# Kernel optimization log

Hardware: AMD Instinct MI355X
Metric: run time of the kernel (lower is better)

## Reference

```python
import jax, jax.numpy as jnp
import numpy as np
from jax import lax

H = 64          # num_heads
P = 64          # head_dim
N = 128         # ssm_state_size
G = 8           # n_groups
K = 4           # conv_kernel
D_MODEL = 4096  # hidden_size
I = H * P                      # intermediate_size = 4096
GN = G * N                     # groups_time_state_size = 1024
CONV_DIM = I + 2 * GN          # 6144
PROJ = I + CONV_DIM + H        # 10304
EPS = 1e-5
GROUP_SIZE = I // G            # 512


def setup_inputs() -> dict:
    key = jax.random.key(0)
    ks = jax.random.split(key, 6)
    B, L = 2, 2048
    s = 0.02
    return {
        "hidden_states": jax.random.normal(ks[0], (B, L, D_MODEL), jnp.float32),
        "in_proj_w": jax.random.normal(ks[1], (PROJ, D_MODEL), jnp.float32) * s,
        "conv_weight": jax.random.normal(ks[2], (CONV_DIM, K), jnp.float32) * s,
        "conv_bias": jnp.zeros((CONV_DIM,), jnp.float32),
        "dt_bias": jnp.ones((H,), jnp.float32),
        "A_log": jnp.log(jnp.arange(1, H + 1, dtype=jnp.float32)),
        "D": jnp.ones((H,), jnp.float32),
        "norm_weight": jnp.ones((I,), jnp.float32),
        "out_proj_w": jax.random.normal(ks[3], (D_MODEL, I), jnp.float32) * s,
    }


def reference(hidden_states, in_proj_w, conv_weight, conv_bias, dt_bias, A_log, D, norm_weight, out_proj_w):
    B, L, _ = hidden_states.shape

    # in_proj, then split into gate / conv-stream / dt
    proj = jnp.einsum("bld,pd->blp", hidden_states, in_proj_w)
    gate = proj[..., :I]
    hbc = proj[..., I:I + CONV_DIM]          # (B, L, conv_dim), pre-conv
    dt = proj[..., -H:]                       # (B, L, H)

    # depthwise causal conv1d + SiLU
    pad = jnp.pad(hbc, ((0, 0), (K - 1, 0), (0, 0)))
    conv = conv_bias
    for k in range(K):  # K=4, tiny fixed loop
        conv = conv + pad[:, k:k + L, :] * conv_weight[:, k]
    xBC = jax.nn.silu(conv)

    x = xBC[..., :I].reshape(B, L, H, P)                        # (B,L,H,P)
    Bm = xBC[..., I:I + GN].reshape(B, L, G, N)
    Cm = xBC[..., I + GN:].reshape(B, L, G, N)
    hpg = H // G
    B_h = jnp.repeat(Bm, hpg, axis=2)                            # (B,L,H,N)
    C_h = jnp.repeat(Cm, hpg, axis=2)                            # (B,L,H,N)

    # dt processing: softplus(dt + dt_bias), limits (0, inf)
    dt_p = jax.nn.softplus(dt + dt_bias)                         # (B,L,H)
    A = -jnp.exp(A_log)                                          # (H,)
    dA = jnp.exp(dt_p * A)                                       # (B,L,H)
    dtx = dt_p[..., None] * x                                    # (B,L,H,P)

    # selective scan over sequence (O(L)), state: (B,H,P,N)
    def step(state, inp):
        dA_t, dtx_t, B_t, C_t = inp
        state = state * dA_t[..., None, None] + dtx_t[..., None] * B_t[:, :, None, :]
        y_t = jnp.einsum("bhpn,bhn->bhp", state, C_t)
        return state, y_t

    xs = (jnp.moveaxis(dA, 1, 0), jnp.moveaxis(dtx, 1, 0),
          jnp.moveaxis(B_h, 1, 0), jnp.moveaxis(C_h, 1, 0))
    state0 = jnp.zeros((B, H, P, N), jnp.float32)
    final_state, ys = lax.scan(step, state0, xs)
    y = jnp.moveaxis(ys, 0, 1) + x * D[None, None, :, None]      # (B,L,H,P)
    y = y.reshape(B, L, I)

    # gated grouped RMSNorm: 8 independent RMSNorms over 512 elems each
    yg = y.reshape(B, L, G, GROUP_SIZE)
    var = jnp.mean(yg * yg, axis=-1, keepdims=True)
    yn = (yg * lax.rsqrt(var + EPS)).reshape(B, L, I) * norm_weight
    yn = yn * jax.nn.silu(gate)

    out = jnp.einsum("bli,di->bld", yn, out_proj_w)

    conv_state_new = jnp.moveaxis(hbc[:, L - (K - 1):, :], 1, 2)  # (B, conv_dim, K-1)
    return out, conv_state_new, final_state
```

## Files before the change

kernel.cpp:

```cpp
#include <hip/hip_runtime.h>
#include <cstdint>
#include <cstddef>

typedef __bf16 bf16;
typedef float f32x4 __attribute__((ext_vector_type(4)));
typedef bf16 bf16x8 __attribute__((ext_vector_type(8)));
typedef bf16 bf16x4 __attribute__((ext_vector_type(4)));

#define DM    4096
#define LL    2048
#define BB    2
#define BT    4096
#define II    4096
#define GN_   1024
#define CONVD 6144
#define PROJD 10304
#define NPAD  10496
#define HH    64
#define PP    64
#define NN    128
#define CT    64
#define NC    32

#define OUT_OFS_CONV  16777216
#define OUT_OFS_STATE 16814080

#define WS_HSB    0UL
#define WS_WINB   33554432UL
#define WS_DSB    0UL
#define WS_PROJ   119537664UL
#define WS_XBC    291504128UL
#define WS_DTDA   392167424UL
#define WS_Y      394264576UL
#define WS_WOUTB  0UL
#define WS_YNB    33554432UL

__device__ __forceinline__ void gl2lds16(const void* g, void* l) {
  __builtin_amdgcn_global_load_lds(
      (__attribute__((address_space(1))) unsigned int*)(uintptr_t)g,
      (__attribute__((address_space(3))) unsigned int*)(uintptr_t)l, 16, 0, 0);
}

__global__ __launch_bounds__(256) void cast_kernel(const float* __restrict__ src,
                                                   bf16* __restrict__ dst,
                                                   long nsrc, long ndst) {
  long i = ((long)blockIdx.x * 256 + threadIdx.x) * 4;
  if (i >= ndst) return;
  bf16x4 o;
  if (i < nsrc) {
    float4 v = *(const float4*)(src + i);
    o[0] = (bf16)v.x; o[1] = (bf16)v.y; o[2] = (bf16)v.z; o[3] = (bf16)v.w;
  } else {
    o[0] = (bf16)0.f; o[1] = (bf16)0.f; o[2] = (bf16)0.f; o[3] = (bf16)0.f;
  }
  *(bf16x4*)(dst + i) = o;
}

#define BARF() do { asm volatile("" ::: "memory");                    \
                    __builtin_amdgcn_s_barrier();                     \
                    asm volatile("" ::: "memory"); } while (0)
#define WAITLGKM0() do { asm volatile("s_waitcnt lgkmcnt(0)" ::: "memory"); \
                         __builtin_amdgcn_sched_barrier(0); } while (0)
#define WAITVM(n) asm volatile("s_waitcnt vmcnt(" #n ")" ::: "memory")
#define PRIO1 __builtin_amdgcn_s_setprio(1)
#define PRIO0 __builtin_amdgcn_s_setprio(0)

__device__ __forceinline__ void stage_A_half(const bf16* __restrict__ A, int K,
                                             int arow, int kt, bf16* lds,
                                             int h, int tid) {
#pragma unroll
  for (int j = 0; j < 2; ++j) {
    const int r  = h * 64 + j * 128 + (tid >> 3);
    const int cb = (tid & 7) * 16;
    const int cs = cb ^ ((r & 7) << 4);
    gl2lds16(A + (size_t)(arow + r) * K + kt * 64 + (cs >> 1),
             lds + r * 64 + (cb >> 1));
  }
}
__device__ __forceinline__ void stage_B_half(const bf16* __restrict__ B, int K,
                                             int brow, int kt, bf16* lds,
                                             int h, int tid) {
#pragma unroll
  for (int j = 0; j < 2; ++j) {
    const int quarter = j * 2 + (tid >> 8);
    const int kq = tid & 255;
    const int r  = quarter * 64 + h * 32 + (kq >> 3);
    const int cb = (kq & 7) * 16;
    const int cs = cb ^ ((r & 7) << 4);
    gl2lds16(B + (size_t)(brow + r) * K + kt * 64 + (cs >> 1),
             lds + r * 64 + (cb >> 1));
  }
}

#define LDA4(p, mh) do {                                                     \
  _Pragma("unroll") for (int mt = 0; mt < 4; ++mt)                           \
  _Pragma("unroll") for (int kk = 0; kk < 2; ++kk) {                         \
    const int rr = wm * 128 + (mh) * 64 + mt * 16 + l16;                     \
    const int cc = (kk * 64 + quad * 16) ^ ((rr & 7) << 4);                  \
    a_[mt][kk] = *(const bf16x8*)((const char*)(&sA[p][rr][0]) + cc);        \
  } } while (0)

#define LDB2(p, np, barr) do {                                               \
  _Pragma("unroll") for (int nt = 0; nt < 2; ++nt)                           \
  _Pragma("unroll") for (int kk = 0; kk < 2; ++kk) {                         \
    const int rr = wn * 64 + (np) * 32 + nt * 16 + l16;                      \
    const int cc = (kk * 64 + quad * 16) ^ ((rr & 7) << 4);                  \
    barr[nt][kk] = *(const bf16x8*)((const char*)(&sB[p][rr][0]) + cc);      \
  } } while (0)

#define MFMAQ(mh, barr, nb0) do {                                            \
  _Pragma("unroll") for (int kk = 0; kk < 2; ++kk)                           \
  _Pragma("unroll") for (int mt = 0; mt < 4; ++mt)                           \
  _Pragma("unroll") for (int nt = 0; nt < 2; ++nt)                           \
    acc[(mh) * 4 + mt][(nb0) + nt] = __builtin_amdgcn_mfma_f32_16x16x32_bf16(\
        a_[mt][kk], barr[nt][kk], acc[(mh) * 4 + mt][(nb0) + nt], 0, 0, 0);  \
  } while (0)

__global__ __launch_bounds__(512, 2) void gemm256(const bf16* __restrict__ A,
                                                  const bf16* __restrict__ B,
                                                  float* __restrict__ C,
                                                  int M, int N, int K, int NB) {
  __shared__ __align__(16) bf16 sA[2][256][64];
  __shared__ __align__(16) bf16 sB[2][256][64];

  const int tid  = threadIdx.x;
  const int wave = tid >> 6, lane = tid & 63;
  const int l16  = lane & 15, quad = lane >> 4;
  const int wm   = wave >> 2, wn = wave & 3;

  const int nwg = gridDim.x;
  const int q = nwg >> 3, r8 = nwg & 7;
  const int xcd = blockIdx.x & 7, idx = blockIdx.x >> 3;
  const int wgid = (xcd < r8 ? xcd * (q + 1) : r8 * (q + 1) + (xcd - r8) * q) + idx;
  const int mb = wgid / NB, nb = wgid - mb * NB;
  const int arow = mb * 256, brow = nb * 256;

  f32x4 acc[8][4];
#pragma unroll
  for (int i = 0; i < 8; ++i)
#pragma unroll
    for (int j = 0; j < 4; ++j) acc[i][j] = (f32x4)0.f;

  const int NT = K >> 6;

  stage_A_half(A, K, arow, 0, &sA[0][0][0], 0, tid);
  stage_B_half(B, K, brow, 0, &sB[0][0][0], 0, tid);
  stage_A_half(A, K, arow, 0, &sA[0][0][0], 1, tid);
  stage_B_half(B, K, brow, 0, &sB[0][0][0], 1, tid);
  stage_A_half(A, K, arow, 1, &sA[1][0][0], 0, tid);
  stage_B_half(B, K, brow, 1, &sB[1][0][0], 0, tid);
  stage_A_half(A, K, arow, 1, &sA[1][0][0], 1, tid);
  WAITVM(6);
  BARF();

  bf16x8 a_[4][2], b0_[2][2], b1_[2][2];

  for (int i = 0; i < NT / 2; ++i) {
    const int t1o = 2 * i + 1;
    const int t2  = (2 * i + 2 < NT) ? 2 * i + 2 : NT - 1;
    const int t3  = (2 * i + 3 < NT) ? 2 * i + 3 : NT - 1;

    LDA4(0, 0); LDB2(0, 0, b0_);
    stage_B_half(B, K, brow, t1o, &sB[1][0][0], 1, tid);
    BARF(); WAITLGKM0();
    PRIO1; MFMAQ(0, b0_, 0); PRIO0;
    BARF();
    LDB2(0, 1, b1_);
    stage_A_half(A, K, arow, t2, &sA[0][0][0], 0, tid);
    BARF(); WAITLGKM0();
    PRIO1; MFMAQ(0, b1_, 2); PRIO0;
    BARF();
    LDA4(0, 1);
    stage_B_half(B, K, brow, t2, &sB[0][0][0], 0, tid);
    BARF(); WAITLGKM0();
    PRIO1; MFMAQ(1, b1_, 2); PRIO0;
    BARF();
    stage_A_half(A, K, arow, t2, &sA[0][0][0], 1, tid);
    WAITVM(6);
    BARF();
    PRIO1; MFMAQ(1, b0_, 0); PRIO0;
    BARF();
    LDA4(1, 0); LDB2(1, 0, b0_);
    stage_B_half(B, K, brow, t2, &sB[0][0][0], 1, tid);
    BARF(); WAITLGKM0();
    PRIO1; MFMAQ(0, b0_, 0); PRIO0;
    BARF();
    LDB2(1, 1, b1_);
    stage_A_half(A, K, arow, t3, &sA[1][0][0], 0, tid);
    BARF(); WAITLGKM0();
    PRIO1; MFMAQ(0, b1_, 2); PRIO0;
    BARF();
    LDA4(1, 1);
    stage_B_half(B, K, brow, t3, &sB[1][0][0], 0, tid);
    BARF(); WAITLGKM0();
    PRIO1; MFMAQ(1, b1_, 2); PRIO0;
    BARF();
    stage_A_half(A, K, arow, t3, &sA[1][0][0], 1, tid);
    WAITVM(6);
    BARF();
    PRIO1; MFMAQ(1, b0_, 0); PRIO0;
    BARF();
  }
  asm volatile("s_waitcnt vmcnt(0)" ::: "memory");
  __builtin_amdgcn_s_barrier();

#pragma unroll
  for (int mt = 0; mt < 8; ++mt) {
    const int row0 = arow + wm * 128 + mt * 16 + quad * 4;
#pragma unroll
    for (int nt = 0; nt < 4; ++nt) {
      const int col = brow + wn * 64 + nt * 16 + l16;
#pragma unroll
      for (int r = 0; r < 4; ++r)
        C[(size_t)(row0 + r) * N + col] = acc[mt][nt][r];
    }
  }
}

#define CTILE 64
__global__ __launch_bounds__(256) void conv_kernel(const float* __restrict__ proj,
                                                   const float* __restrict__ cw,
                                                   const float* __restrict__ cb,
                                                   bf16* __restrict__ xbc) {
  const int c   = blockIdx.x * 256 + threadIdx.x;
  const int bt0 = blockIdx.y * CTILE;
  const int t0  = bt0 & (LL - 1);
  const float4 w = *(const float4*)(cw + c * 4);
  const float bias = cb[c];
  const float* p = proj + (size_t)bt0 * NPAD + II + c;
  float h0, h1, h2;
  if (t0 == 0) {
    h0 = 0.f; h1 = 0.f; h2 = 0.f;
  } else {
    h0 = p[-3 * (ptrdiff_t)NPAD];
    h1 = p[-2 * (ptrdiff_t)NPAD];
    h2 = p[-(ptrdiff_t)NPAD];
  }
  bf16* q = xbc + (size_t)bt0 * CONVD + c;
#pragma unroll 8
  for (int t = 0; t < CTILE; ++t) {
    const float cur = p[(ptrdiff_t)t * NPAD];
    const float acc = bias + h0 * w.x + h1 * w.y + h2 * w.z + cur * w.w;
    q[(size_t)t * CONVD] = (bf16)(acc / (1.f + __expf(-acc)));
    h0 = h1; h1 = h2; h2 = cur;
  }
}

__global__ __launch_bounds__(256) void dt_kernel(const float* __restrict__ proj,
                                                 const float* __restrict__ dt_bias,
                                                 const float* __restrict__ A_log,
                                                 float* __restrict__ dtda) {
  const int idx = blockIdx.x * 256 + threadIdx.x;
  const int bt = idx >> 6, h = idx & 63;
  const float z = proj[(size_t)bt * NPAD + (II + CONVD) + h] + dt_bias[h];
  const float sp = (z > 20.f) ? z : log1pf(__expf(z));
  const float a = -__expf(A_log[h]);
  float2 o; o.x = sp; o.y = __expf(sp * a);
  *(float2*)(dtda + (size_t)idx * 2) = o;
}

__global__ __launch_bounds__(256) void convstate_kernel(const float* __restrict__ proj,
                                                        float* __restrict__ outp) {
  const int idx = blockIdx.x * 256 + threadIdx.x;
  if (idx >= BB * CONVD * 3) return;
  const int b = idx / (CONVD * 3);
  const int r = idx - b * CONVD * 3;
  const int c = r / 3, j = r - c * 3;
  outp[idx] = proj[((size_t)b * LL + (LL - 3 + j)) * NPAD + II + c];
}

__global__ __launch_bounds__(256) void chunkA_kernel(const bf16* __restrict__ xbc,
                                                     const float* __restrict__ dtda,
                                                     const float* __restrict__ A_log,
                                                     float* __restrict__ ybuf,
                                                     bf16* __restrict__ dsb) {
  const int h = blockIdx.x, c = blockIdx.y, b = blockIdx.z;
  const int g = h >> 3;
  const int tid = threadIdx.x;
  const int wave = tid >> 6, lane = tid & 63;
  const int l16 = lane & 15, quad = lane >> 4;

  __shared__ __align__(16) bf16 CsBt[8192];
  __shared__ __align__(16) bf16 Bs[64][128];
  __shared__ __align__(16) bf16 Xt[64][64];
  __shared__ __align__(16) bf16 Ws[64][64];
  __shared__ float cums[64], dtps[64], wls[64];

  bf16 (*Cs)[128] = (bf16(*)[128])CsBt;
  bf16 (*Bt)[64]  = (bf16(*)[64])CsBt;

  const size_t rowbase = ((size_t)b * LL + (size_t)c * CT) * CONVD;

  {
    const int i = tid >> 2, col0 = (tid & 3) * 32;
    const bf16* gpC = xbc + rowbase + (size_t)i * CONVD + (II + GN_) + g * 128 + col0;
    const bf16* gpB = xbc + rowbase + (size_t)i * CONVD + II + g * 128 + col0;
    const int sx = i & 15;
#pragma unroll
    for (int k = 0; k < 4; ++k) {
      const int n0 = col0 + k * 8;
      const int eo = ((n0 >> 3) ^ sx) * 8;
      *(bf16x8*)(&Cs[i][0] + eo) = *(const bf16x8*)(gpC + k * 8);
      *(bf16x8*)(&Bs[i][0] + eo) = *(const bf16x8*)(gpB + k * 8);
    }
  }
  {
    const int j = tid >> 2, p0 = (tid & 3) * 16;
    const bf16* gpX = xbc + rowbase + (size_t)j * CONVD + h * 64 + p0;
#pragma unroll
    for (int k = 0; k < 2; ++k) {
      bf16x8 v = *(const bf16x8*)(gpX + k * 8);
#pragma unroll
      for (int e = 0; e < 8; ++e) {
        const int pp = p0 + k * 8 + e;
        Xt[pp][(((j >> 3) ^ (pp & 7)) * 8) + (j & 7)] = v[e];
      }
    }
  }
  if (wave == 0) {
    const float Ah = -__expf(A_log[h]);
    float2 dd = *(const float2*)(dtda + ((size_t)((b * LL + c * CT + lane)) * 64 + h) * 2);
    float s = dd.x * Ah;
#pragma unroll
    for (int d = 1; d < 64; d <<= 1) {
      float v = __shfl_up(s, d);
      if (lane >= d) s += v;
    }
    const float tot = __shfl(s, 63);
    cums[lane] = s;
    dtps[lane] = dd.x;
    wls[lane]  = __expf(tot - s) * dd.x;
  }
  __syncthreads();

  const int mrow = wave * 16 + l16;
  {
    f32x4 accg[4];
#pragma unroll
    for (int nt = 0; nt < 4; ++nt) accg[nt] = (f32x4)0.f;
#pragma unroll
    for (int k0 = 0; k0 < 128; k0 += 32) {
      bf16x8 af = *(const bf16x8*)&Cs[mrow][(((k0 >> 3) + quad) ^ (mrow & 15)) * 8];
#pragma unroll
      for (int nt = 0; nt < 4; ++nt) {
        const int nrow = nt * 16 + l16;
        bf16x8 bfr = *(const bf16x8*)&Bs[nrow][(((k0 >> 3) + quad) ^ (nrow & 15)) * 8];
        accg[nt] = __builtin_amdgcn_mfma_f32_16x16x32_bf16(af, bfr, accg[nt], 0, 0, 0);
      }
    }
#pragma unroll
    for (int nt = 0; nt < 4; ++nt) {
      const int j = nt * 16 + l16;
#pragma unroll
      for (int r = 0; r < 4; ++r) {
        const int i = wave * 16 + quad * 4 + r;
        float v = 0.f;
        if (j <= i) v = accg[nt][r] * __expf(cums[i] - cums[j]) * dtps[j];
        Ws[i][(((j >> 3) ^ (i & 7)) * 8) + (j & 7)] = (bf16)v;
      }
    }
  }
  __syncthreads();

  {
    const int n = tid >> 1, j0 = (tid & 1) * 32;
#pragma unroll
    for (int jj = 0; jj < 32; ++jj) {
      const int j = j0 + jj;
      bf16 v = Bs[j][(((n >> 3) ^ (j & 15)) * 8) + (n & 7)];
      Bt[n][(((j >> 3) ^ (n & 7)) * 8) + (j & 7)] = v;
    }
  }
  __syncthreads();

  f32x4 accy[4];
#pragma unroll
  for (int pt = 0; pt < 4; ++pt) accy[pt] = (f32x4)0.f;
#pragma unroll
  for (int k0 = 0; k0 < 64; k0 += 32) {
    bf16x8 af = *(const bf16x8*)&Ws[mrow][(((k0 >> 3) + quad) ^ (mrow & 7)) * 8];
#pragma unroll
    for (int pt = 0; pt < 4; ++pt) {
      const int prow = pt * 16 + l16;
      bf16x8 bfr = *(const bf16x8*)&Xt[prow][(((k0 >> 3) + quad) ^ (prow & 7)) * 8];
      accy[pt] = __builtin_amdgcn_mfma_f32_16x16x32_bf16(af, bfr, accy[pt], 0, 0, 0);
    }
  }

  f32x4 accs[8];
#pragma unroll
  for (int nt = 0; nt < 8; ++nt) accs[nt] = (f32x4)0.f;
#pragma unroll
  for (int k0 = 0; k0 < 64; k0 += 32) {
    bf16x8 axr = *(const bf16x8*)&Xt[mrow][(((k0 >> 3) + quad) ^ (mrow & 7)) * 8];
    bf16x8 ax;
#pragma unroll
    for (int e = 0; e < 8; ++e)
      ax[e] = (bf16)((float)axr[e] * wls[k0 + quad * 8 + e]);
#pragma unroll
    for (int nt = 0; nt < 8; ++nt) {
      const int nrow = nt * 16 + l16;
      bf16x8 bfr = *(const bf16x8*)&Bt[nrow][(((k0 >> 3) + quad) ^ (nrow & 7)) * 8];
      accs[nt] = __builtin_amdgcn_mfma_f32_16x16x32_bf16(ax, bfr, accs[nt], 0, 0, 0);
    }
  }

#pragma unroll
  for (int pt = 0; pt < 4; ++pt) {
#pragma unroll
    for (int r = 0; r < 4; ++r) {
      const int i = wave * 16 + quad * 4 + r;
      ybuf[((size_t)(b * LL + c * CT + i)) * II + h * 64 + pt * 16 + l16] = accy[pt][r];
    }
  }
  const size_t dbase = (((size_t)(b * HH + h)) * NC + c) * (CT * NN);
#pragma unroll
  for (int nt = 0; nt < 8; ++nt) {
#pragma unroll
    for (int r = 0; r < 4; ++r) {
      const int p = wave * 16 + quad * 4 + r;
      dsb[dbase + (size_t)p * NN + nt * 16 + l16] = (bf16)accs[nt][r];
    }
  }
}

__global__ __launch_bounds__(256) void chain_kernel(const float* __restrict__ dtda,
                                                    const float* __restrict__ A_log,
                                                    bf16* __restrict__ dsb,
                                                    float* __restrict__ fst) {
  const int blk = blockIdx.x;
  const int b = blk >> 8, h = (blk >> 2) & 63, qtr = blk & 3;
  const int tid = threadIdx.x, wave = tid >> 6, lane = tid & 63;
  __shared__ float DcL[NC];

  const float Ah = -__expf(A_log[h]);
#pragma unroll
  for (int cc = 0; cc < 8; ++cc) {
    const int c = wave * 8 + cc;
    float2 dd = *(const float2*)(dtda + ((size_t)(b * LL + c * CT + lane) * 64 + h) * 2);
    float a = dd.x * Ah;
#pragma unroll
    for (int m = 1; m <= 32; m <<= 1) a += __shfl_xor(a, m);
    if (lane == 0) DcL[c] = __expf(a);
  }
  __syncthreads();

  const int local = qtr * 2048 + tid * 8;
  const size_t base = ((size_t)(b * HH + h)) * NC * (CT * NN) + local;
  float s[8];
#pragma unroll
  for (int e = 0; e < 8; ++e) s[e] = 0.f;

  for (int c = 0; c < NC; ++c) {
    bf16* p = dsb + base + (size_t)c * (CT * NN);
    bf16x8 d0 = *(const bf16x8*)(p);
    const float dc = DcL[c];
    bf16x8 o0;
#pragma unroll
    for (int e = 0; e < 8; ++e) o0[e] = (bf16)s[e];
    *(bf16x8*)(p) = o0;
#pragma unroll
    for (int e = 0; e < 8; ++e) s[e] = s[e] * dc + (float)d0[e];
  }
  float* fp = fst + ((size_t)(b * HH + h)) * (PP * NN) + local;
#pragma unroll
  for (int k = 0; k < 2; ++k) {
    float4 v = { s[k * 4], s[k * 4 + 1], s[k * 4 + 2], s[k * 4 + 3] };
    *(float4*)(fp + k * 4) = v;
  }
}

__global__ __launch_bounds__(256) void chunkB_kernel(const bf16* __restrict__ xbc,
                                                     const float* __restrict__ dtda,
                                                     const float* __restrict__ A_log,
                                                     const float* __restrict__ Dv,
                                                     const bf16* __restrict__ spb,
                                                     float* __restrict__ ybuf) {
  const int h = blockIdx.x, c = blockIdx.y, b = blockIdx.z;
  const int g = h >> 3;
  const int tid = threadIdx.x;
  const int wave = tid >> 6, lane = tid & 63;
  const int l16 = lane & 15, quad = lane >> 4;

  __shared__ __align__(16) bf16 Cs[64][128];
  __shared__ __align__(16) bf16 Sp[64][128];
  __shared__ float es[64];

  const size_t rowbase = ((size_t)b * LL + (size_t)c * CT) * CONVD;
  {
    const int i = tid >> 2, col0 = (tid & 3) * 32;
    const bf16* gpC = xbc + rowbase + (size_t)i * CONVD + (II + GN_) + g * 128 + col0;
    const int sx = i & 15;
#pragma unroll
    for (int k = 0; k < 4; ++k) {
      const int n0 = col0 + k * 8;
      *(bf16x8*)(&Cs[i][0] + (((n0 >> 3) ^ sx) * 8)) = *(const bf16x8*)(gpC + k * 8);
    }
  }
  {
    const int p = tid >> 2, nseg = (tid & 3) * 32;
    const bf16* gp = spb + (((size_t)(b * HH + h)) * NC + c) * (CT * NN) + (size_t)p * NN + nseg;
    const int sx = p & 15;
#pragma unroll
    for (int k = 0; k < 4; ++k) {
      const int n0 = nseg + k * 8;
      bf16x8 v = *(const bf16x8*)(gp + k * 8);
      *(bf16x8*)(&Sp[p][0] + (((n0 >> 3) ^ sx) * 8)) = v;
    }
  }
  if (wave == 0) {
    const float Ah = -__expf(A_log[h]);
    float2 dd = *(const float2*)(dtda + ((size_t)(b * LL + c * CT + lane) * 64 + h) * 2);
    float s = dd.x * Ah;
#pragma unroll
    for (int d = 1; d < 64; d <<= 1) {
      float v = __shfl_up(s, d);
      if (lane >= d) s += v;
    }
    es[lane] = __expf(s);
  }
  __syncthreads();

  const int mrow = wave * 16 + l16;
  f32x4 acc[4];
#pragma unroll
  for (int pt = 0; pt < 4; ++pt) acc[pt] = (f32x4)0.f;
#pragma unroll
  for (int k0 = 0; k0 < 128; k0 += 32) {
    bf16x8 af = *(const bf16x8*)&Cs[mrow][(((k0 >> 3) + quad) ^ (mrow & 15)) * 8];
#pragma unroll
    for (int pt = 0; pt < 4; ++pt) {
      const int prow = pt * 16 + l16;
      bf16x8 bfr = *(const bf16x8*)&Sp[prow][(((k0 >> 3) + quad) ^ (prow & 15)) * 8];
      acc[pt] = __builtin_amdgcn_mfma_f32_16x16x32_bf16(af, bfr, acc[pt], 0, 0, 0);
    }
  }

  const float Dh = Dv[h];
#pragma unroll
  for (int pt = 0; pt < 4; ++pt) {
#pragma unroll
    for (int r = 0; r < 4; ++r) {
      const int i = wave * 16 + quad * 4 + r;
      const int p = pt * 16 + l16;
      const size_t row = (size_t)(b * LL + c * CT + i);
      const size_t ya = row * II + h * 64 + p;
      const float xv = (float)xbc[row * CONVD + h * 64 + p];
      ybuf[ya] = acc[pt][r] * es[i] + ybuf[ya] + Dh * xv;
    }
  }
}

__global__ __launch_bounds__(256) void norm_kernel(const float* __restrict__ y,
                                                   const float* __restrict__ proj,
                                                   const float* __restrict__ nw,
                                                   bf16* __restrict__ yn) {
  const int bt = blockIdx.x, tid = threadIdx.x;
  const float* yr = y + (size_t)bt * II + tid * 16;
  float4 v[4];
  float ss = 0.f;
#pragma unroll
  for (int i = 0; i < 4; ++i) {
    v[i] = *(const float4*)(yr + i * 4);
    ss += v[i].x * v[i].x + v[i].y * v[i].y + v[i].z * v[i].z + v[i].w * v[i].w;
  }
#pragma unroll
  for (int m = 1; m <= 16; m <<= 1) ss += __shfl_xor(ss, m);
  const float rstd = rsqrtf(ss * (1.f / 512.f) + 1e-5f);

  const float* gr  = proj + (size_t)bt * NPAD + tid * 16;
  const float* nwr = nw + tid * 16;
  bf16x8 o0, o1;
#pragma unroll
  for (int i = 0; i < 4; ++i) {
    float4 gv = *(const float4*)(gr + i * 4);
    float4 nv = *(const float4*)(nwr + i * 4);
    const float* vv = (const float*)&v[i];
    const float* gg = (const float*)&gv;
    const float* nn = (const float*)&nv;
#pragma unroll
    for (int j = 0; j < 4; ++j) {
      const float gate = gg[j];
      const float val = vv[j] * rstd * nn[j] * (gate / (1.f + __expf(-gate)));
      if (i < 2) o0[i * 4 + j] = (bf16)val;
      else       o1[(i - 2) * 4 + j] = (bf16)val;
    }
  }
  bf16* dst = yn + (size_t)bt * II + tid * 16;
  *(bf16x8*)(dst)     = o0;
  *(bf16x8*)(dst + 8) = o1;
}

extern "C" void kernel_launch(void* const* d_in, const int* in_sizes, int n_in,
                              void* d_out, int out_size, void* d_ws, size_t ws_size,
                              hipStream_t stream) {
  const float* hs      = (const float*)d_in[0];
  const float* w_in    = (const float*)d_in[1];
  const float* cw      = (const float*)d_in[2];
  const float* cb      = (const float*)d_in[3];
  const float* dt_bias = (const float*)d_in[4];
  const float* A_log   = (const float*)d_in[5];
  const float* Dv      = (const float*)d_in[6];
  const float* nw      = (const float*)d_in[7];
  const float* w_out   = (const float*)d_in[8];

  char* ws = (char*)d_ws;
  bf16*  hsb   = (bf16*)(ws + WS_HSB);
  bf16*  winb  = (bf16*)(ws + WS_WINB);
  bf16*  dsb   = (bf16*)(ws + WS_DSB);
  float* proj  = (float*)(ws + WS_PROJ);
  bf16*  xbc   = (bf16*)(ws + WS_XBC);
  float* dtda  = (float*)(ws + WS_DTDA);
  float* ybuf  = (float*)(ws + WS_Y);
  bf16*  ynb   = (bf16*)(ws + WS_YNB);
  bf16*  woutb = (bf16*)(ws + WS_WOUTB);

  float* outp = (float*)d_out;

  cast_kernel<<<16384, 256, 0, stream>>>(hs, hsb, 16777216L, 16777216L);
  cast_kernel<<<41984, 256, 0, stream>>>(w_in, winb, (long)PROJD * DM, (long)NPAD * DM);

  gemm256<<<(BT / 256) * (NPAD / 256), 512, 0, stream>>>(hsb, winb, proj, BT, NPAD, DM, NPAD / 256);

  conv_kernel<<<dim3(CONVD / 256, BT / CTILE), 256, 0, stream>>>(proj, cw, cb, xbc);
  dt_kernel<<<(BT * HH) / 256, 256, 0, stream>>>(proj, dt_bias, A_log, dtda);
  convstate_kernel<<<(BB * CONVD * 3 + 255) / 256, 256, 0, stream>>>(proj, outp + OUT_OFS_CONV);

  chunkA_kernel<<<dim3(HH, NC, BB), 256, 0, stream>>>(xbc, dtda, A_log, ybuf, dsb);
  chain_kernel<<<BB * HH * 4, 256, 0, stream>>>(dtda, A_log, dsb, outp + OUT_OFS_STATE);
  chunkB_kernel<<<dim3(HH, NC, BB), 256, 0, stream>>>(xbc, dtda, A_log, Dv, dsb, ybuf);

  cast_kernel<<<16384, 256, 0, stream>>>(w_out, woutb, 16777216L, 16777216L);
  norm_kernel<<<BT, 256, 0, stream>>>(ybuf, proj, nw, ynb);

  gemm256<<<(BT / 256) * (DM / 256), 512, 0, stream>>>(ynb, woutb, outp, BT, DM, II, DM / 256);
}
```

Baseline: 974.2 us.

## Merge small kernels, remap scan blocks for L2 locality, use direct-to-LDS loads

Combines the two input casts into one launch and merges the dt and conv-state kernels, which cuts launch overhead. The chunk kernels now use a 1D grid decoded so blocks that share a group's B/C data run near each other, for better L2 reuse. Their B/C and state staging now goes through global_load_lds, and the B transpose writes 8-element vectors. The chain kernel prefetches the next chunk's state, and the GEMM gets an extra lgkmcnt wait hint. Several unrelated tweaks together, each with a small effect and some risk around LDS swizzle correctness.

```diff
diff --git a/kernel.cpp b/kernel.cpp
--- a/kernel.cpp
+++ b/kernel.cpp
@@ -41,6 +41,31 @@
       (__attribute__((address_space(3))) unsigned int*)(uintptr_t)l, 16, 0, 0);
 }
 
+__global__ __launch_bounds__(256) void cast2_kernel(const float* __restrict__ s1,
+                                                    bf16* __restrict__ d1,
+                                                    const float* __restrict__ s2,
+                                                    bf16* __restrict__ d2,
+                                                    long nsrc2, long ndst2) {
+  if (blockIdx.x < 16384) {
+    long i = ((long)blockIdx.x * 256 + threadIdx.x) * 4;
+    float4 v = *(const float4*)(s1 + i);
+    bf16x4 o;
+    o[0] = (bf16)v.x; o[1] = (bf16)v.y; o[2] = (bf16)v.z; o[3] = (bf16)v.w;
+    *(bf16x4*)(d1 + i) = o;
+  } else {
+    long i = ((long)(blockIdx.x - 16384) * 256 + threadIdx.x) * 4;
+    if (i >= ndst2) return;
+    bf16x4 o;
+    if (i < nsrc2) {
+      float4 v = *(const float4*)(s2 + i);
+      o[0] = (bf16)v.x; o[1] = (bf16)v.y; o[2] = (bf16)v.z; o[3] = (bf16)v.w;
+    } else {
+      o[0] = (bf16)0.f; o[1] = (bf16)0.f; o[2] = (bf16)0.f; o[3] = (bf16)0.f;
+    }
+    *(bf16x4*)(d2 + i) = o;
+  }
+}
+
 __global__ __launch_bounds__(256) void cast_kernel(const float* __restrict__ src,
                                                    bf16* __restrict__ dst,
                                                    long nsrc, long ndst) {
@@ -61,6 +86,7 @@
                     asm volatile("" ::: "memory"); } while (0)
 #define WAITLGKM0() do { asm volatile("s_waitcnt lgkmcnt(0)" ::: "memory"); \
                          __builtin_amdgcn_sched_barrier(0); } while (0)
+#define HINTLGKM8() asm volatile("s_waitcnt lgkmcnt(8)" ::: "memory")
 #define WAITVM(n) asm volatile("s_waitcnt vmcnt(" #n ")" ::: "memory")
 #define PRIO1 __builtin_amdgcn_s_setprio(1)
 #define PRIO0 __builtin_amdgcn_s_setprio(0)
@@ -162,6 +188,7 @@
 
     LDA4(0, 0); LDB2(0, 0, b0_);
     stage_B_half(B, K, brow, t1o, &sB[1][0][0], 1, tid);
+    HINTLGKM8();
     BARF(); WAITLGKM0();
     PRIO1; MFMAQ(0, b0_, 0); PRIO0;
     BARF();
@@ -182,6 +209,7 @@
     BARF();
     LDA4(1, 0); LDB2(1, 0, b0_);
     stage_B_half(B, K, brow, t2, &sB[0][0][0], 1, tid);
+    HINTLGKM8();
     BARF(); WAITLGKM0();
     PRIO1; MFMAQ(0, b0_, 0); PRIO0;
     BARF();
@@ -246,36 +274,43 @@
   }
 }
 
-__global__ __launch_bounds__(256) void dt_kernel(const float* __restrict__ proj,
-                                                 const float* __restrict__ dt_bias,
-                                                 const float* __restrict__ A_log,
-                                                 float* __restrict__ dtda) {
-  const int idx = blockIdx.x * 256 + threadIdx.x;
-  const int bt = idx >> 6, h = idx & 63;
-  const float z = proj[(size_t)bt * NPAD + (II + CONVD) + h] + dt_bias[h];
-  const float sp = (z > 20.f) ? z : log1pf(__expf(z));
-  const float a = -__expf(A_log[h]);
-  float2 o; o.x = sp; o.y = __expf(sp * a);
-  *(float2*)(dtda + (size_t)idx * 2) = o;
-}
-
-__global__ __launch_bounds__(256) void convstate_kernel(const float* __restrict__ proj,
-                                                        float* __restrict__ outp) {
-  const int idx = blockIdx.x * 256 + threadIdx.x;
-  if (idx >= BB * CONVD * 3) return;
-  const int b = idx / (CONVD * 3);
-  const int r = idx - b * CONVD * 3;
-  const int c = r / 3, j = r - c * 3;
-  outp[idx] = proj[((size_t)b * LL + (LL - 3 + j)) * NPAD + II + c];
-}
+__global__ __launch_bounds__(256) void dtcs_kernel(const float* __restrict__ proj,
+                                                   const float* __restrict__ dt_bias,
+                                                   const float* __restrict__ A_log,
+                                                   float* __restrict__ dtda,
+                                                   float* __restrict__ outp) {
+  const int bid = blockIdx.x;
+  if (bid < 1024) {
+    const int idx = bid * 256 + threadIdx.x;
+    const int bt = idx >> 6, h = idx & 63;
+    const float z = proj[(size_t)bt * NPAD + (II + CONVD) + h] + dt_bias[h];
+    const float sp = (z > 20.f) ? z : log1pf(__expf(z));
+    const float a = -__expf(A_log[h]);
+    float2 o; o.x = sp; o.y = __expf(sp * a);
+    *(float2*)(dtda + (size_t)idx * 2) = o;
+  } else {
+    const int idx = (bid - 1024) * 256 + threadIdx.x;
+    if (idx >= BB * CONVD * 3) return;
+    const int b = idx / (CONVD * 3);
+    const int r = idx - b * CONVD * 3;
+    const int c = r / 3, j = r - c * 3;
+    outp[idx] = proj[((size_t)b * LL + (LL - 3 + j)) * NPAD + II + c];
+  }
+}
+
+#define SCAN_DECODE()                                                  \
+  const int lin = blockIdx.x;                                          \
+  const int hh  = (lin >> 3) & 7;                                      \
+  const int id  = (lin & 7) | ((lin >> 6) << 3);                       \
+  const int g   = id >> 6, c = (id >> 1) & 31, b = id & 1;             \
+  const int h   = g * 8 + hh;
 
 __global__ __launch_bounds__(256) void chunkA_kernel(const bf16* __restrict__ xbc,
                                                      const float* __restrict__ dtda,
                                                      const float* __restrict__ A_log,
                                                      float* __restrict__ ybuf,
                                                      bf16* __restrict__ dsb) {
-  const int h = blockIdx.x, c = blockIdx.y, b = blockIdx.z;
-  const int g = h >> 3;
+  SCAN_DECODE();
   const int tid = threadIdx.x;
   const int wave = tid >> 6, lane = tid & 63;
   const int l16 = lane & 15, quad = lane >> 4;
@@ -292,16 +327,15 @@
   const size_t rowbase = ((size_t)b * LL + (size_t)c * CT) * CONVD;
 
   {
-    const int i = tid >> 2, col0 = (tid & 3) * 32;
-    const bf16* gpC = xbc + rowbase + (size_t)i * CONVD + (II + GN_) + g * 128 + col0;
-    const bf16* gpB = xbc + rowbase + (size_t)i * CONVD + II + g * 128 + col0;
-    const int sx = i & 15;
-#pragma unroll
-    for (int k = 0; k < 4; ++k) {
-      const int n0 = col0 + k * 8;
-      const int eo = ((n0 >> 3) ^ sx) * 8;
-      *(bf16x8*)(&Cs[i][0] + eo) = *(const bf16x8*)(gpC + k * 8);
-      *(bf16x8*)(&Bs[i][0] + eo) = *(const bf16x8*)(gpB + k * 8);
+    const int r0 = wave * 16;
+    const bf16* gC = xbc + rowbase + (II + GN_) + g * 128;
+    const bf16* gB = xbc + rowbase + II + g * 128;
+#pragma unroll
+    for (int j = 0; j < 4; ++j) {
+      const int r  = r0 + j * 4 + (lane >> 4);
+      const int ch = (lane & 15) ^ (r & 15);
+      gl2lds16(gC + (size_t)r * CONVD + ch * 8, &Cs[r0 + j * 4][0]);
+      gl2lds16(gB + (size_t)r * CONVD + ch * 8, &Bs[r0 + j * 4][0]);
     }
   }
   {
@@ -365,10 +399,14 @@
   {
     const int n = tid >> 1, j0 = (tid & 1) * 32;
 #pragma unroll
-    for (int jj = 0; jj < 32; ++jj) {
-      const int j = j0 + jj;
-      bf16 v = Bs[j][(((n >> 3) ^ (j & 15)) * 8) + (n & 7)];
-      Bt[n][(((j >> 3) ^ (n & 7)) * 8) + (j & 7)] = v;
+    for (int k = 0; k < 4; ++k) {
+      bf16x8 v;
+#pragma unroll
+      for (int e = 0; e < 8; ++e) {
+        const int j = j0 + k * 8 + e;
+        v[e] = Bs[j][(((n >> 3) ^ (j & 15)) * 8) + (n & 7)];
+      }
+      *(bf16x8*)(&Bt[n][((((j0 + k * 8) >> 3) ^ (n & 7)) * 8)]) = v;
     }
   }
   __syncthreads();
@@ -443,7 +481,6 @@
     for (int m = 1; m <= 32; m <<= 1) a += __shfl_xor(a, m);
     if (lane == 0) DcL[c] = __expf(a);
   }
-  __syncthreads();
 
   const int local = qtr * 2048 + tid * 8;
   const size_t base = ((size_t)(b * HH + h)) * NC * (CT * NN) + local;
@@ -451,9 +488,13 @@
 #pragma unroll
   for (int e = 0; e < 8; ++e) s[e] = 0.f;
 
+  bf16x8 d0 = *(const bf16x8*)(dsb + base);
+  __syncthreads();
+
   for (int c = 0; c < NC; ++c) {
     bf16* p = dsb + base + (size_t)c * (CT * NN);
-    bf16x8 d0 = *(const bf16x8*)(p);
+    bf16x8 dn;
+    if (c + 1 < NC) dn = *(const bf16x8*)(p + (CT * NN));
     const float dc = DcL[c];
     bf16x8 o0;
 #pragma unroll
@@ -461,6 +502,7 @@
     *(bf16x8*)(p) = o0;
 #pragma unroll
     for (int e = 0; e < 8; ++e) s[e] = s[e] * dc + (float)d0[e];
+    d0 = dn;
   }
   float* fp = fst + ((size_t)(b * HH + h)) * (PP * NN) + local;
 #pragma unroll
@@ -476,8 +518,7 @@
                                                      const float* __restrict__ Dv,
                                                      const bf16* __restrict__ spb,
                                                      float* __restrict__ ybuf) {
-  const int h = blockIdx.x, c = blockIdx.y, b = blockIdx.z;
-  const int g = h >> 3;
+  SCAN_DECODE();
   const int tid = threadIdx.x;
   const int wave = tid >> 6, lane = tid & 63;
   const int l16 = lane & 15, quad = lane >> 4;
@@ -488,24 +529,15 @@
 
   const size_t rowbase = ((size_t)b * LL + (size_t)c * CT) * CONVD;
   {
-    const int i = tid >> 2, col0 = (tid & 3) * 32;
-    const bf16* gpC = xbc + rowbase + (size_t)i * CONVD + (II + GN_) + g * 128 + col0;
-    const int sx = i & 15;
-#pragma unroll
-    for (int k = 0; k < 4; ++k) {
-      const int n0 = col0 + k * 8;
-      *(bf16x8*)(&Cs[i][0] + (((n0 >> 3) ^ sx) * 8)) = *(const bf16x8*)(gpC + k * 8);
-    }
-  }
-  {
-    const int p = tid >> 2, nseg = (tid & 3) * 32;
-    const bf16* gp = spb + (((size_t)(b * HH + h)) * NC + c) * (CT * NN) + (size_t)p * NN + nseg;
-    const int sx = p & 15;
-#pragma unroll
-    for (int k = 0; k < 4; ++k) {
-      const int n0 = nseg + k * 8;
-      bf16x8 v = *(const bf16x8*)(gp + k * 8);
-      *(bf16x8*)(&Sp[p][0] + (((n0 >> 3) ^ sx) * 8)) = v;
+    const int r0 = wave * 16;
+    const bf16* gC = xbc + rowbase + (II + GN_) + g * 128;
+    const bf16* gS = spb + (((size_t)(b * HH + h)) * NC + c) * (CT * NN);
+#pragma unroll
+    for (int j = 0; j < 4; ++j) {
+      const int r  = r0 + j * 4 + (lane >> 4);
+      const int ch = (lane & 15) ^ (r & 15);
+      gl2lds16(gC + (size_t)r * CONVD + ch * 8, &Cs[r0 + j * 4][0]);
+      gl2lds16(gS + (size_t)r * NN   + ch * 8, &Sp[r0 + j * 4][0]);
     }
   }
   if (wave == 0) {
@@ -617,18 +649,17 @@
 
   float* outp = (float*)d_out;
 
-  cast_kernel<<<16384, 256, 0, stream>>>(hs, hsb, 16777216L, 16777216L);
-  cast_kernel<<<41984, 256, 0, stream>>>(w_in, winb, (long)PROJD * DM, (long)NPAD * DM);
+  cast2_kernel<<<58368, 256, 0, stream>>>(hs, hsb, w_in, winb,
+                                          (long)PROJD * DM, (long)NPAD * DM);
 
   gemm256<<<(BT / 256) * (NPAD / 256), 512, 0, stream>>>(hsb, winb, proj, BT, NPAD, DM, NPAD / 256);
 
   conv_kernel<<<dim3(CONVD / 256, BT / CTILE), 256, 0, stream>>>(proj, cw, cb, xbc);
-  dt_kernel<<<(BT * HH) / 256, 256, 0, stream>>>(proj, dt_bias, A_log, dtda);
-  convstate_kernel<<<(BB * CONVD * 3 + 255) / 256, 256, 0, stream>>>(proj, outp + OUT_OFS_CONV);
-
-  chunkA_kernel<<<dim3(HH, NC, BB), 256, 0, stream>>>(xbc, dtda, A_log, ybuf, dsb);
+  dtcs_kernel<<<1168, 256, 0, stream>>>(proj, dt_bias, A_log, dtda, outp + OUT_OFS_CONV);
+
+  chunkA_kernel<<<4096, 256, 0, stream>>>(xbc, dtda, A_log, ybuf, dsb);
   chain_kernel<<<BB * HH * 4, 256, 0, stream>>>(dtda, A_log, dsb, outp + OUT_OFS_STATE);
-  chunkB_kernel<<<dim3(HH, NC, BB), 256, 0, stream>>>(xbc, dtda, A_log, Dv, dsb, ybuf);
+  chunkB_kernel<<<4096, 256, 0, stream>>>(xbc, dtda, A_log, Dv, dsb, ybuf);
 
   cast_kernel<<<16384, 256, 0, stream>>>(w_out, woutb, 16777216L, 16777216L);
   norm_kernel<<<BT, 256, 0, stream>>>(ybuf, proj, nw, ynb);
```

New measurement: 962.2 us. Within noise of the previous version (-1.2%).
